# Kernel optimization log

Measured on AMD Instinct MI355X. Metric: run time of the kernel, lower is better.

Reference implementation:

```python
import jax, jax.numpy as jnp
import numpy as np

L, B, S, D, H, F = 4, 8, 512, 512, 8, 2048
KS = (1, 3, 5)
DEPTH = D // H


def causal_conv(x, W, b):
    # x: [B,S,D], W: [k,D,D] (WIO), causal left pad k-1
    k = W.shape[0]
    y = jax.lax.conv_general_dilated(x, W, (1,), [(k - 1, 0)],
                                     dimension_numbers=('NWC', 'WIO', 'NWC'))
    return y + b


def layer_norm(x, g, b, eps=1e-6):
    mu = jnp.mean(x, -1, keepdims=True)
    var = jnp.mean((x - mu) ** 2, -1, keepdims=True)
    return (x - mu) * jax.lax.rsqrt(var + eps) * g + b


def split_heads(t):
    return t.reshape(B, S, H, DEPTH).transpose(0, 2, 1, 3)  # [B,H,S,depth]


def setup_inputs() -> dict:
    key = jax.random.key(0)
    keys = iter(jax.random.split(key, 16))
    rn = lambda shape, s=0.02: jax.random.normal(next(keys), shape, jnp.float32) * s
    inp = {"x": jax.random.normal(next(keys), (B, S, D), jnp.float32)}
    for k in KS:
        inp[f"Wq{k}"] = rn((L, k, D, D))
        inp[f"Wk{k}"] = rn((L, k, D, D))
    inp["bq"] = jnp.zeros((L, 3, D), jnp.float32)
    inp["bk"] = jnp.zeros((L, 3, D), jnp.float32)
    inp["Wv"] = rn((L, 3, 1, D, D))
    inp["bv"] = jnp.zeros((L, 3, D), jnp.float32)
    inp["Wo"] = rn((L, D, D)); inp["bo"] = jnp.zeros((L, D), jnp.float32)
    inp["W1"] = rn((L, D, F)); inp["b1"] = jnp.zeros((L, F), jnp.float32)
    inp["W2"] = rn((L, F, D)); inp["b2"] = jnp.zeros((L, D), jnp.float32)
    inp["ln1_g"] = jnp.ones((L, D), jnp.float32); inp["ln1_b"] = jnp.zeros((L, D), jnp.float32)
    inp["ln2_g"] = jnp.ones((L, D), jnp.float32); inp["ln2_b"] = jnp.zeros((L, D), jnp.float32)
    return inp


def reference(x, Wq1, Wq3, Wq5, Wk1, Wk3, Wk5, bq, bk, Wv, bv, Wo, bo,
              W1, b1, W2, b2, ln1_g, ln1_b, ln2_g, ln2_b):
    # causal look-ahead mask: 1 - band_part(ones, -1, 0), added as mask * -1e9
    neg_mask = (1.0 - jnp.tril(jnp.ones((S, S), jnp.float32))) * -1e9
    scale = 1.0 / jnp.sqrt(jnp.float32(DEPTH))
    Wqs, Wks = (Wq1, Wq3, Wq5), (Wk1, Wk3, Wk5)
    for l in range(L):
        outs = []
        for i in range(len(KS)):
            q = split_heads(causal_conv(x, Wqs[i][l], bq[l, i]))
            k = split_heads(causal_conv(x, Wks[i][l], bk[l, i]))
            v = split_heads(causal_conv(x, Wv[l, i], bv[l, i]))
            logits = jnp.einsum('bhqd,bhkd->bhqk', q, k) * scale + neg_mask
            a = jax.nn.softmax(logits, axis=-1)
            o = jnp.einsum('bhqk,bhkd->bhqd', a, v)
            outs.append(o.transpose(0, 2, 1, 3).reshape(B, S, D))
        attn_out = ((outs[0] + outs[1] + outs[2]) / 3.0) @ Wo[l] + bo[l]
        out1 = layer_norm(attn_out + x, ln1_g[l], ln1_b[l])
        ffn = jax.nn.relu(out1 @ W1[l] + b1[l]) @ W2[l] + b2[l]
        x = layer_norm(ffn + out1, ln2_g[l], ln2_b[l])
    return x
```

## Files before the change

kernel.cpp:

```cpp
#include <hip/hip_runtime.h>
#include <cstdint>
#include <cstddef>

#define Dm 512
#define Sm 512
#define Bm 8
#define Hm 8
#define Fm 2048
#define Mm 4096
#define Lm 4

typedef __bf16 bf16x8 __attribute__((ext_vector_type(8)));
typedef float  fx4    __attribute__((ext_vector_type(4)));
typedef float  fx2    __attribute__((ext_vector_type(2)));
typedef unsigned short u16;
typedef unsigned short u16x4 __attribute__((ext_vector_type(4)));
typedef short s16x8 __attribute__((ext_vector_type(8)));

__device__ __forceinline__ u16 f2b(float f) {
  union { float f; uint32_t u; } v; v.f = f;
  uint32_t u = v.u;
  return (u16)((u + 0x7fffu + ((u >> 16) & 1u)) >> 16);
}
__device__ __forceinline__ float b2f(u16 h) {
  union { uint32_t u; float f; } v; v.u = ((uint32_t)h) << 16;
  return v.f;
}

__device__ __forceinline__ void gload16(const void* g, void* l) {
  __builtin_amdgcn_global_load_lds(
      (const __attribute__((address_space(1))) void*)g,
      (__attribute__((address_space(3))) void*)l, 16, 0, 0);
}

__global__ void cast_bf16_kernel(const float* __restrict__ in, u16* __restrict__ out,
                                 u16* __restrict__ zpad) {
  int i = (blockIdx.x * 256 + threadIdx.x) * 4;
  fx4 v = *(const fx4*)(in + i);
  u16x4 o;
  #pragma unroll
  for (int j = 0; j < 4; ++j) o[j] = f2b(v[j]);
  *(u16x4*)(out + i) = o;
  if (blockIdx.x == 0) { zpad[threadIdx.x] = 0; zpad[threadIdx.x + 256] = 0; }
}

__global__ void avg3_kernel(const u16* __restrict__ o3, u16* __restrict__ out) {
  int i = (blockIdx.x * 256 + threadIdx.x) * 4;
  u16x4 a = *(const u16x4*)(o3 + i);
  u16x4 b = *(const u16x4*)(o3 + (size_t)Mm*Dm + i);
  u16x4 c = *(const u16x4*)(o3 + (size_t)2*Mm*Dm + i);
  u16x4 r;
  #pragma unroll
  for (int j = 0; j < 4; ++j)
    r[j] = f2b((b2f(a[j]) + b2f(b[j]) + b2f(c[j])) * (1.f/3.f));
  *(u16x4*)(out + i) = r;
}

__global__ void ln_kernel(const float* __restrict__ in, const float* __restrict__ gam,
                          const float* __restrict__ bet, float* __restrict__ outf,
                          u16* __restrict__ outb) {
  int row = blockIdx.x;
  int t = threadIdx.x;
  const float* x = in + (size_t)row * Dm;
  fx4 v0 = *(const fx4*)(x + t*4);
  fx4 v1 = *(const fx4*)(x + 256 + t*4);
  float s = 0.f, sq = 0.f;
  #pragma unroll
  for (int j = 0; j < 4; ++j) { s += v0[j] + v1[j]; sq += v0[j]*v0[j] + v1[j]*v1[j]; }
  #pragma unroll
  for (int off = 1; off < 64; off <<= 1) { s += __shfl_xor(s, off, 64); sq += __shfl_xor(sq, off, 64); }
  float mu  = s * (1.f/Dm);
  float var = sq * (1.f/Dm) - mu*mu;
  float rstd = rsqrtf(var + 1e-6f);
  fx4 g0 = *(const fx4*)(gam + t*4), g1 = *(const fx4*)(gam + 256 + t*4);
  fx4 b0 = *(const fx4*)(bet + t*4), b1 = *(const fx4*)(bet + 256 + t*4);
  float* of = outf + (size_t)row*Dm;
  u16*   ob = outb + (size_t)row*Dm;
  fx4 y0, y1; u16x4 h0, h1;
  #pragma unroll
  for (int j = 0; j < 4; ++j) {
    y0[j] = (v0[j]-mu)*rstd*g0[j] + b0[j];
    y1[j] = (v1[j]-mu)*rstd*g1[j] + b1[j];
    h0[j] = f2b(y0[j]); h1[j] = f2b(y1[j]);
  }
  *(fx4*)(of + t*4) = y0; *(fx4*)(of + 256 + t*4) = y1;
  *(u16x4*)(ob + t*4) = h0; *(u16x4*)(ob + 256 + t*4) = h1;
}

#define TST 130
__global__ void prep_kernel(u16* __restrict__ packed,
    const float* __restrict__ Wq1, const float* __restrict__ Wq3, const float* __restrict__ Wq5,
    const float* __restrict__ Wk1, const float* __restrict__ Wk3, const float* __restrict__ Wk5,
    const float* __restrict__ Wv,  const float* __restrict__ Wo,
    const float* __restrict__ W1,  const float* __restrict__ W2, int layer) {
  __shared__ float T[64 * TST];
  constexpr int t0[13] = {0,32,128,288,320,416,576,608,640,672,704,832,960};
  int bid = blockIdx.x;
  int seg = 0;
  while (bid >= t0[seg+1]) ++seg;
  int local = bid - t0[seg];
  const float* src; int K, N;
  switch (seg) {
    case 0:  src = Wq1 + (size_t)layer*512*512;   K = 512;  N = 512;  break;
    case 1:  src = Wq3 + (size_t)layer*3*512*512; K = 1536; N = 512;  break;
    case 2:  src = Wq5 + (size_t)layer*5*512*512; K = 2560; N = 512;  break;
    case 3:  src = Wk1 + (size_t)layer*512*512;   K = 512;  N = 512;  break;
    case 4:  src = Wk3 + (size_t)layer*3*512*512; K = 1536; N = 512;  break;
    case 5:  src = Wk5 + (size_t)layer*5*512*512; K = 2560; N = 512;  break;
    case 6:  src = Wv + (size_t)(layer*3+0)*512*512; K = 512; N = 512; break;
    case 7:  src = Wv + (size_t)(layer*3+1)*512*512; K = 512; N = 512; break;
    case 8:  src = Wv + (size_t)(layer*3+2)*512*512; K = 512; N = 512; break;
    case 9:  src = Wo + (size_t)layer*512*512;    K = 512;  N = 512;  break;
    case 10: src = W1 + (size_t)layer*512*2048;   K = 512;  N = 2048; break;
    default: src = W2 + (size_t)layer*2048*512;   K = 2048; N = 512;  break;
  }
  int KT = K >> 6;
  int ntile = local / KT, ktile = local - ntile*KT;
  const float* sb = src + (size_t)(ktile*64)*N + ntile*128;
  int tid = threadIdx.x;
  #pragma unroll
  for (int i = 0; i < 16; ++i) {
    int idx = i*256 + tid;
    int row = idx >> 6, col2 = (idx & 63) * 2;
    fx2 v = *(const fx2*)(sb + (size_t)row*N + col2);
    *(fx2*)(&T[row*TST + col2]) = v;
  }
  __syncthreads();
  u16* dst = packed + ((size_t)bid << 13);
  #pragma unroll
  for (int j = 0; j < 4; ++j) {
    int z = j*256 + tid;
    int row = z >> 3;
    int c = (z & 7) ^ (row & 7);
    s16x8 o;
    #pragma unroll
    for (int e = 0; e < 8; ++e) o[e] = (short)f2b(T[(c*8 + e)*TST + row]);
    *(s16x8*)(dst + z*8) = o;
  }
}

__global__ __launch_bounds__(256, 2) void conv_all(const u16* __restrict__ xb,
    const u16* __restrict__ packed,
    const float* __restrict__ bq, const float* __restrict__ bk, const float* __restrict__ bv,
    u16* __restrict__ qb, u16* __restrict__ kb, u16* __restrict__ vT, int layer,
    const u16* __restrict__ zpad) {
  __shared__ __align__(16) u16 As[2][8192];
  __shared__ __align__(16) u16 Bs[2][8192];
  constexpr int t0c[9]   = {0,32,128,288,320,416,576,608,640};
  constexpr int tapsc[9] = {1,3,5,1,3,5,1,1,1};
  constexpr int order[9] = {2,5,1,4,0,3,6,7,8};
  int bid = blockIdx.x;
  int unit = order[bid >> 7];
  int local = bid & 127;
  int mtile = local >> 2, ntile = local & 3;
  int taps = tapsc[unit];
  int brow = mtile * 128, bcol = ntile * 128;
  int tid = threadIdx.x, lane = tid & 63, wid = tid >> 6;
  int wm = wid >> 1, wn = wid & 1;
  int r16 = lane & 15, g = lane >> 4;
  int tbase = t0c[unit] + ntile * taps * 8;
  fx4 acc[4][4] = {};
  int ntiles = taps * 8;
  int st = 0, skt = 0, sidx = 0;
  auto stage = [&](int bufi) {
    int shift = taps - 1 - st;
    int c0 = skt << 6;
    #pragma unroll
    for (int j = 0; j < 4; ++j) {
      int zb = wid*256 + j*64;
      int zz = zb + lane;
      int row = zz >> 3, c = (zz & 7) ^ (row & 7);
      int s = (brow + row) & (Sm - 1);
      const u16* src = (s >= shift) ? (xb + (size_t)(brow + row - shift)*Dm + c0 + c*8) : zpad;
      gload16(src, &As[bufi][zb * 8]);
    }
    const u16* wt = packed + ((size_t)(tbase + sidx) << 13);
    #pragma unroll
    for (int j = 0; j < 4; ++j) {
      int zb = wid*256 + j*64;
      gload16(wt + (size_t)(zb + lane)*8, &Bs[bufi][zb * 8]);
    }
  };
  stage(0);
  ++skt; ++sidx; if (skt == 8) { skt = 0; ++st; }
  __syncthreads();
  for (int idx = 0; idx < ntiles; ++idx) {
    int cur = idx & 1;
    if (idx + 1 < ntiles) {
      stage(cur ^ 1);
      ++skt; ++sidx; if (skt == 8) { skt = 0; ++st; }
    }
    bf16x8 a[2][4], b[2][4];
    #pragma unroll
    for (int kk = 0; kk < 2; ++kk) {
      #pragma unroll
      for (int m = 0; m < 4; ++m) {
        int row = wm*64 + m*16 + r16;
        a[kk][m] = *(const bf16x8*)(&As[cur][(row << 6) + (((kk*4 + g) ^ (row & 7)) << 3)]);
      }
      #pragma unroll
      for (int n = 0; n < 4; ++n) {
        int row = wn*64 + n*16 + r16;
        b[kk][n] = *(const bf16x8*)(&Bs[cur][(row << 6) + (((kk*4 + g) ^ (row & 7)) << 3)]);
      }
    }
    #pragma unroll
    for (int kk = 0; kk < 2; ++kk)
      #pragma unroll
      for (int m = 0; m < 4; ++m)
        #pragma unroll
        for (int n = 0; n < 4; ++n)
          acc[m][n] = __builtin_amdgcn_mfma_f32_16x16x32_bf16(a[kk][m], b[kk][n], acc[m][n], 0, 0, 0);
    __syncthreads();
  }
  const float* bias; u16* outp;
  if (unit < 3)      { bias = bq + (size_t)(layer*3 + unit)*Dm;   outp = qb + (size_t)unit*Mm*Dm; }
  else if (unit < 6) { bias = bk + (size_t)(layer*3 + unit-3)*Dm; outp = kb + (size_t)(unit-3)*Mm*Dm; }
  else               { bias = bv + (size_t)(layer*3 + unit-6)*Dm; outp = vT + ((size_t)(unit-6) << 21); }
  if (unit < 6) {
    #pragma unroll
    for (int m = 0; m < 4; ++m) {
      int row0 = brow + wm*64 + m*16 + g*4;
      #pragma unroll
      for (int n = 0; n < 4; ++n) {
        int col = bcol + wn*64 + n*16 + r16;
        float bv_ = bias[col];
        #pragma unroll
        for (int r = 0; r < 4; ++r)
          outp[(size_t)(row0 + r)*Dm + col] = f2b(acc[m][n][r] + bv_);
      }
    }
  } else {
    #pragma unroll
    for (int m = 0; m < 4; ++m) {
      int row0 = brow + wm*64 + m*16 + g*4;
      int bidx = row0 >> 9, spos = row0 & 511;
      #pragma unroll
      for (int n = 0; n < 4; ++n) {
        int col = bcol + wn*64 + n*16 + r16;
        int hh = col >> 6, dd = col & 63;
        float bv_ = bias[col];
        u16x4 pk;
        #pragma unroll
        for (int r = 0; r < 4; ++r) pk[r] = f2b(acc[m][n][r] + bv_);
        *(u16x4*)(outp + (((size_t)(bidx*8 + hh)*64 + dd) << 9) + spos) = pk;
      }
    }
  }
}

template<int MODE, int BMt, int WN, bool CAUSAL>
__device__ __forceinline__ void gemm_core(const u16* __restrict__ A, int lda, int Ktap, int taps,
    const u16* __restrict__ Wt, const float* __restrict__ bias, const float* __restrict__ res,
    u16* __restrict__ outb, float* __restrict__ outf, int N, const u16* __restrict__ zpad) {
  constexpr int NR = 128 / (16 * WN);
  __shared__ __align__(16) u16 As[2][BMt * 64];
  __shared__ __align__(16) u16 Bs[2][8192];
  int tid = threadIdx.x, lane = tid & 63, wid = tid >> 6;
  int wm = (WN == 2) ? (wid >> 1) : 0;
  int wn = (WN == 2) ? (wid & 1) : wid;
  int r16 = lane & 15, g = lane >> 4;
  int brow = blockIdx.x * BMt, bcol = blockIdx.y * 128;
  int KT = Ktap >> 6;
  const u16* WtN = Wt + ((size_t)(blockIdx.y * taps * KT) << 13);
  fx4 acc[4][NR] = {};
  int ntiles = taps * KT;
  int st = 0, skt = 0, sidx = 0;
  auto stage = [&](int bufi) {
    int shift = taps - 1 - st;
    int c0 = skt << 6;
    #pragma unroll
    for (int j = 0; j < BMt/32; ++j) {
      int zb = wid*(BMt*2) + j*64;
      int zz = zb + lane;
      int row = zz >> 3, c = (zz & 7) ^ (row & 7);
      const u16* src;
      if (CAUSAL) {
        int s = (brow + row) & (Sm - 1);
        src = (s >= shift) ? (A + (size_t)(brow + row - shift)*lda + c0 + c*8) : zpad;
      } else {
        src = A + (size_t)(brow + row)*lda + c0 + c*8;
      }
      gload16(src, &As[bufi][zb * 8]);
    }
    const u16* wt = WtN + ((size_t)sidx << 13);
    #pragma unroll
    for (int j = 0; j < 4; ++j) {
      int zb = wid*256 + j*64;
      gload16(wt + (size_t)(zb + lane)*8, &Bs[bufi][zb * 8]);
    }
  };
  stage(0);
  ++skt; ++sidx; if (skt == KT) { skt = 0; ++st; }
  __syncthreads();
  for (int idx = 0; idx < ntiles; ++idx) {
    int cur = idx & 1;
    if (idx + 1 < ntiles) {
      stage(cur ^ 1);
      ++skt; ++sidx; if (skt == KT) { skt = 0; ++st; }
    }
    bf16x8 a[2][4], b[2][NR];
    #pragma unroll
    for (int kk = 0; kk < 2; ++kk) {
      #pragma unroll
      for (int m = 0; m < 4; ++m) {
        int row = wm*64 + m*16 + r16;
        a[kk][m] = *(const bf16x8*)(&As[cur][(row << 6) + (((kk*4 + g) ^ (row & 7)) << 3)]);
      }
      #pragma unroll
      for (int n = 0; n < NR; ++n) {
        int row = wn*(NR*16) + n*16 + r16;
        b[kk][n] = *(const bf16x8*)(&Bs[cur][(row << 6) + (((kk*4 + g) ^ (row & 7)) << 3)]);
      }
    }
    #pragma unroll
    for (int kk = 0; kk < 2; ++kk)
      #pragma unroll
      for (int m = 0; m < 4; ++m)
        #pragma unroll
        for (int n = 0; n < NR; ++n)
          acc[m][n] = __builtin_amdgcn_mfma_f32_16x16x32_bf16(a[kk][m], b[kk][n], acc[m][n], 0, 0, 0);
    __syncthreads();
  }
  #pragma unroll
  for (int m = 0; m < 4; ++m) {
    int row0 = brow + wm*64 + m*16 + g*4;
    #pragma unroll
    for (int n = 0; n < NR; ++n) {
      int col = bcol + wn*(NR*16) + n*16 + r16;
      float bv_ = bias[col];
      #pragma unroll
      for (int r = 0; r < 4; ++r) {
        size_t idx = (size_t)(row0 + r)*N + col;
        float v = acc[m][n][r] + bv_;
        if (MODE == 0)      outb[idx] = f2b(v);
        else if (MODE == 1) outb[idx] = f2b(fmaxf(v, 0.f));
        else                outf[idx] = v + res[idx];
      }
    }
  }
}

template<int MODE, int BMt, int WN, int LB>
__global__ __launch_bounds__(256, LB) void gemm_dense(const u16* __restrict__ A, int lda, int K,
    const u16* __restrict__ Wt, const float* __restrict__ bias, const float* __restrict__ res,
    u16* __restrict__ outb, float* __restrict__ outf, int N) {
  gemm_core<MODE, BMt, WN, false>(A, lda, K, 1, Wt, bias, res, outb, outf, N, nullptr);
}

__global__ __launch_bounds__(256, 3) void attn_kernel(const u16* __restrict__ qb,
    const u16* __restrict__ kb, const u16* __restrict__ vTb, u16* __restrict__ ob) {
  __shared__ __align__(16) u16 Ks[2][4096];
  __shared__ __align__(16) u16 Vs[2][4096];
  __shared__ __align__(16) u16 Ps[4][1024];
  int a = blockIdx.x, bh = blockIdx.y, br = blockIdx.z;
  int b = bh >> 3, h = bh & 7;
  const u16* q  = qb + (size_t)br*Mm*Dm;
  const u16* k  = kb + (size_t)br*Mm*Dm;
  const u16* vT = vTb + (((size_t)br << 21) + ((size_t)bh << 15));
  u16* o = ob + (size_t)br*Mm*Dm;
  int tid = threadIdx.x, lane = tid & 63, wid = tid >> 6;
  int r16 = lane & 15, g = lane >> 4;
  size_t rowbase = (size_t)b * Sm;
  int qt[2] = {7 - a, a};
  int nkt = qt[0] + 1;

  bf16x8 qa[2][2];
  #pragma unroll
  for (int t2 = 0; t2 < 2; ++t2)
    #pragma unroll
    for (int c = 0; c < 2; ++c)
      qa[t2][c] = *(const bf16x8*)(q + (rowbase + qt[t2]*64 + wid*16 + r16)*Dm + h*64 + c*32 + g*8);

  float m_[2][4], l_[2][4];
  fx4 accO[2][4] = {};
  #pragma unroll
  for (int t2 = 0; t2 < 2; ++t2)
    #pragma unroll
    for (int r = 0; r < 4; ++r) { m_[t2][r] = -3.0e38f; l_[t2][r] = 0.f; }

  auto stage = [&](int kt, int bufi) {
    #pragma unroll
    for (int it = 0; it < 2; ++it) {
      int zb = wid*128 + it*64;
      int zz = zb + lane;
      int row = zz >> 3, c = (zz & 7) ^ (row & 7);
      gload16(k + (rowbase + kt*64 + row)*Dm + h*64 + c*8, &Ks[bufi][zb * 8]);
      gload16(vT + ((size_t)row << 9) + kt*64 + c*8, &Vs[bufi][zb * 8]);
    }
  };
  stage(0, 0);
  __syncthreads();

  for (int kt = 0; kt < nkt; ++kt) {
    int cur = kt & 1;
    if (kt + 1 < nkt) stage(kt + 1, cur ^ 1);
    #pragma unroll
    for (int t2 = 0; t2 < 2; ++t2) {
      if (t2 == 0 || kt <= qt[1]) {
        fx4 sacc[4] = {};
        #pragma unroll
        for (int c = 0; c < 2; ++c)
          #pragma unroll
          for (int n = 0; n < 4; ++n) {
            int row = n*16 + r16;
            bf16x8 kf = *(const bf16x8*)(&Ks[cur][(row << 6) + (((c*4 + g) ^ (row & 7)) << 3)]);
            sacc[n] = __builtin_amdgcn_mfma_f32_16x16x32_bf16(qa[t2][c], kf, sacc[n], 0, 0, 0);
          }
        float sv[4][4];
        bool diag = (kt == qt[t2]);
        #pragma unroll
        for (int n = 0; n < 4; ++n)
          #pragma unroll
          for (int r = 0; r < 4; ++r) {
            float s = sacc[n][r] * 0.125f;
            if (diag && (n*16 + r16 > wid*16 + g*4 + r)) s = -3.0e38f;
            sv[n][r] = s;
          }
        #pragma unroll
        for (int r = 0; r < 4; ++r) {
          float rm = fmaxf(fmaxf(sv[0][r], sv[1][r]), fmaxf(sv[2][r], sv[3][r]));
          #pragma unroll
          for (int off = 1; off < 16; off <<= 1) rm = fmaxf(rm, __shfl_xor(rm, off, 64));
          float mnew = fmaxf(m_[t2][r], rm);
          float corr = __expf(m_[t2][r] - mnew);
          m_[t2][r] = mnew;
          float rs = 0.f;
          #pragma unroll
          for (int n = 0; n < 4; ++n) { float p = __expf(sv[n][r] - mnew); sv[n][r] = p; rs += p; }
          #pragma unroll
          for (int off = 1; off < 16; off <<= 1) rs += __shfl_xor(rs, off, 64);
          l_[t2][r] = l_[t2][r]*corr + rs;
          #pragma unroll
          for (int n = 0; n < 4; ++n) accO[t2][n][r] *= corr;
        }
        #pragma unroll
        for (int n = 0; n < 4; ++n)
          #pragma unroll
          for (int r = 0; r < 4; ++r) {
            int qq = g*4 + r;
            Ps[wid][(qq << 6) + (((n*2 + (r16 >> 3)) ^ (qq & 7)) << 3) + (r16 & 7)] = f2b(sv[n][r]);
          }
        #pragma unroll
        for (int kk = 0; kk < 2; ++kk) {
          bf16x8 pa = *(const bf16x8*)(&Ps[wid][(r16 << 6) + (((kk*4 + g) ^ (r16 & 7)) << 3)]);
          #pragma unroll
          for (int n = 0; n < 4; ++n) {
            int row = n*16 + r16;
            bf16x8 vf = *(const bf16x8*)(&Vs[cur][(row << 6) + (((kk*4 + g) ^ (row & 7)) << 3)]);
            accO[t2][n] = __builtin_amdgcn_mfma_f32_16x16x32_bf16(pa, vf, accO[t2][n], 0, 0, 0);
          }
        }
      }
    }
    __syncthreads();
  }
  #pragma unroll
  for (int t2 = 0; t2 < 2; ++t2)
    #pragma unroll
    for (int n = 0; n < 4; ++n)
      #pragma unroll
      for (int r = 0; r < 4; ++r) {
        int qrow = qt[t2]*64 + wid*16 + g*4 + r;
        o[(rowbase + qrow)*Dm + h*64 + n*16 + r16] = f2b(accO[t2][n][r] / l_[t2][r]);
      }
}

extern "C" void kernel_launch(void* const* d_in, const int* in_sizes, int n_in,
                              void* d_out, int out_size, void* d_ws, size_t ws_size,
                              hipStream_t stream) {
  const float* x_in = (const float*)d_in[0];
  const float* Wq1 = (const float*)d_in[1];
  const float* Wk1 = (const float*)d_in[2];
  const float* Wq3 = (const float*)d_in[3];
  const float* Wk3 = (const float*)d_in[4];
  const float* Wq5 = (const float*)d_in[5];
  const float* Wk5 = (const float*)d_in[6];
  const float* bq  = (const float*)d_in[7];
  const float* bk  = (const float*)d_in[8];
  const float* Wv  = (const float*)d_in[9];
  const float* bv  = (const float*)d_in[10];
  const float* Wo  = (const float*)d_in[11];
  const float* bo  = (const float*)d_in[12];
  const float* W1  = (const float*)d_in[13];
  const float* b1  = (const float*)d_in[14];
  const float* W2  = (const float*)d_in[15];
  const float* b2  = (const float*)d_in[16];
  const float* ln1g = (const float*)d_in[17];
  const float* ln1b = (const float*)d_in[18];
  const float* ln2g = (const float*)d_in[19];
  const float* ln2b = (const float*)d_in[20];

  char* ws = (char*)d_ws;
  size_t off = 0;
  auto alloc = [&](size_t bytes) { void* p = ws + off; off += (bytes + 255) & ~(size_t)255; return p; };
  float* x_f32 = (float*)alloc((size_t)Mm*Dm*4);
  u16*   xb    = (u16*)  alloc((size_t)Mm*Dm*2);
  u16*   qbuf  = (u16*)  alloc((size_t)3*Mm*Dm*2);
  u16*   kbuf  = (u16*)  alloc((size_t)3*Mm*Dm*2);
  u16*   vT    = (u16*)  alloc((size_t)3*Mm*Dm*2);
  u16*   obuf  = (u16*)  alloc((size_t)3*Mm*Dm*2);
  u16*   avgb  = (u16*)  alloc((size_t)Mm*Dm*2);
  float* pre   = (float*)alloc((size_t)Mm*Dm*4);
  float* out1f = (float*)alloc((size_t)Mm*Dm*4);
  u16*   out1b = (u16*)  alloc((size_t)Mm*Dm*2);
  u16*   midb  = (u16*)  alloc((size_t)Mm*Fm*2);
  u16*   packed= (u16*)  alloc((size_t)960*8192*2);
  u16*   zpad  = (u16*)  alloc(1024);

  cast_bf16_kernel<<<2048, 256, 0, stream>>>(x_in, xb, zpad);
  for (int l = 0; l < Lm; ++l) {
    const float* xs = (l == 0) ? x_in : x_f32;
    prep_kernel<<<960, 256, 0, stream>>>(packed, Wq1, Wq3, Wq5, Wk1, Wk3, Wk5,
                                         Wv, Wo, W1, W2, l);
    conv_all<<<1152, 256, 0, stream>>>(
        xb, packed, bq, bk, bv, qbuf, kbuf, vT, l, zpad);
    attn_kernel<<<dim3(4, 64, 3), 256, 0, stream>>>(qbuf, kbuf, vT, obuf);
    avg3_kernel<<<2048, 256, 0, stream>>>(obuf, avgb);
    gemm_dense<2, 64, 4, 3><<<dim3(64, 4), 256, 0, stream>>>(
        avgb, 512, 512, packed + ((size_t)672 << 13), bo + (size_t)l*Dm, xs, nullptr, pre, 512);
    ln_kernel<<<4096, 64, 0, stream>>>(pre, ln1g + (size_t)l*Dm, ln1b + (size_t)l*Dm, out1f, out1b);
    gemm_dense<1, 128, 2, 2><<<dim3(32, 16), 256, 0, stream>>>(
        out1b, 512, 512, packed + ((size_t)704 << 13), b1 + (size_t)l*Fm, nullptr, midb, nullptr, 2048);
    gemm_dense<2, 64, 4, 3><<<dim3(64, 4), 256, 0, stream>>>(
        midb, 2048, 2048, packed + ((size_t)832 << 13), b2 + (size_t)l*Dm, out1f, nullptr, pre, 512);
    float* lnout = (l == Lm-1) ? (float*)d_out : x_f32;
    ln_kernel<<<4096, 64, 0, stream>>>(pre, ln2g + (size_t)l*Dm, ln2b + (size_t)l*Dm, lnout, xb);
  }
}
```

Measured before the change: 649.2 us.

## Read weight tiles straight from global memory and split FFN2 K across two partial outputs

The conv and GEMM kernels no longer stage the packed weight (B) tiles through shared memory. Each wave loads its B fragments directly from global memory, relying on cache reuse. This halves LDS use so occupancy can rise, and the launch bounds move to 3 blocks per SM. The FFN2 GEMM is split-K into two halves written to separate fp32 buffers, which the following LayerNorm sums, doubling grid size. The risk is global-load latency on B that is no longer hidden by a double buffer, plus extra fp32 traffic for the second partial buffer.

Measured after the change: 671.4 us. +3.4%, slower.

```diff
diff --git a/kernel.cpp b/kernel.cpp
--- a/kernel.cpp
+++ b/kernel.cpp
@@ -34,7 +34,7 @@
 }
 
 __global__ void cast_bf16_kernel(const float* __restrict__ in, u16* __restrict__ out,
-                                 u16* __restrict__ zpad) {
+                                 u16* __restrict__ zpad, float* __restrict__ zerof) {
   int i = (blockIdx.x * 256 + threadIdx.x) * 4;
   fx4 v = *(const fx4*)(in + i);
   u16x4 o;
@@ -42,6 +42,10 @@
   for (int j = 0; j < 4; ++j) o[j] = f2b(v[j]);
   *(u16x4*)(out + i) = o;
   if (blockIdx.x == 0) { zpad[threadIdx.x] = 0; zpad[threadIdx.x + 256] = 0; }
+  if (blockIdx.x == 1) {
+    #pragma unroll
+    for (int j = 0; j < 8; ++j) zerof[threadIdx.x * 8 + j] = 0.f;
+  }
 }
 
 __global__ void avg3_kernel(const u16* __restrict__ o3, u16* __restrict__ out) {
@@ -56,14 +60,21 @@
   *(u16x4*)(out + i) = r;
 }
 
-__global__ void ln_kernel(const float* __restrict__ in, const float* __restrict__ gam,
-                          const float* __restrict__ bet, float* __restrict__ outf,
-                          u16* __restrict__ outb) {
+__global__ void ln_kernel(const float* __restrict__ in, const float* __restrict__ in2,
+                          const float* __restrict__ gam, const float* __restrict__ bet,
+                          float* __restrict__ outf, u16* __restrict__ outb) {
   int row = blockIdx.x;
   int t = threadIdx.x;
   const float* x = in + (size_t)row * Dm;
   fx4 v0 = *(const fx4*)(x + t*4);
   fx4 v1 = *(const fx4*)(x + 256 + t*4);
+  if (in2) {
+    const float* x2 = in2 + (size_t)row * Dm;
+    fx4 w0 = *(const fx4*)(x2 + t*4);
+    fx4 w1 = *(const fx4*)(x2 + 256 + t*4);
+    #pragma unroll
+    for (int j = 0; j < 4; ++j) { v0[j] += w0[j]; v1[j] += w1[j]; }
+  }
   float s = 0.f, sq = 0.f;
   #pragma unroll
   for (int j = 0; j < 4; ++j) { s += v0[j] + v1[j]; sq += v0[j]*v0[j] + v1[j]*v1[j]; }
@@ -139,13 +150,12 @@
   }
 }
 
-__global__ __launch_bounds__(256, 2) void conv_all(const u16* __restrict__ xb,
+__global__ __launch_bounds__(256, 3) void conv_all(const u16* __restrict__ xb,
     const u16* __restrict__ packed,
     const float* __restrict__ bq, const float* __restrict__ bk, const float* __restrict__ bv,
     u16* __restrict__ qb, u16* __restrict__ kb, u16* __restrict__ vT, int layer,
     const u16* __restrict__ zpad) {
   __shared__ __align__(16) u16 As[2][8192];
-  __shared__ __align__(16) u16 Bs[2][8192];
   constexpr int t0c[9]   = {0,32,128,288,320,416,576,608,640};
   constexpr int tapsc[9] = {1,3,5,1,3,5,1,1,1};
   constexpr int order[9] = {2,5,1,4,0,3,6,7,8};
@@ -161,8 +171,8 @@
   int tbase = t0c[unit] + ntile * taps * 8;
   fx4 acc[4][4] = {};
   int ntiles = taps * 8;
-  int st = 0, skt = 0, sidx = 0;
-  auto stage = [&](int bufi) {
+  int st = 0, skt = 0;
+  auto stageA = [&](int bufi) {
     int shift = taps - 1 - st;
     int c0 = skt << 6;
     #pragma unroll
@@ -174,36 +184,33 @@
       const u16* src = (s >= shift) ? (xb + (size_t)(brow + row - shift)*Dm + c0 + c*8) : zpad;
       gload16(src, &As[bufi][zb * 8]);
     }
-    const u16* wt = packed + ((size_t)(tbase + sidx) << 13);
-    #pragma unroll
-    for (int j = 0; j < 4; ++j) {
-      int zb = wid*256 + j*64;
-      gload16(wt + (size_t)(zb + lane)*8, &Bs[bufi][zb * 8]);
-    }
   };
-  stage(0);
-  ++skt; ++sidx; if (skt == 8) { skt = 0; ++st; }
+  stageA(0);
+  ++skt; if (skt == 8) { skt = 0; ++st; }
   __syncthreads();
   for (int idx = 0; idx < ntiles; ++idx) {
     int cur = idx & 1;
+    const u16* wtc = packed + ((size_t)(tbase + idx) << 13);
+    bf16x8 b[2][4];
+    #pragma unroll
+    for (int kk = 0; kk < 2; ++kk)
+      #pragma unroll
+      for (int n = 0; n < 4; ++n) {
+        int row = wn*64 + n*16 + r16;
+        b[kk][n] = *(const bf16x8*)(wtc + (row << 6) + (((kk*4 + g) ^ (row & 7)) << 3));
+      }
     if (idx + 1 < ntiles) {
-      stage(cur ^ 1);
-      ++skt; ++sidx; if (skt == 8) { skt = 0; ++st; }
-    }
-    bf16x8 a[2][4], b[2][4];
-    #pragma unroll
-    for (int kk = 0; kk < 2; ++kk) {
+      stageA(cur ^ 1);
+      ++skt; if (skt == 8) { skt = 0; ++st; }
+    }
+    bf16x8 a[2][4];
+    #pragma unroll
+    for (int kk = 0; kk < 2; ++kk)
       #pragma unroll
       for (int m = 0; m < 4; ++m) {
         int row = wm*64 + m*16 + r16;
         a[kk][m] = *(const bf16x8*)(&As[cur][(row << 6) + (((kk*4 + g) ^ (row & 7)) << 3)]);
       }
-      #pragma unroll
-      for (int n = 0; n < 4; ++n) {
-        int row = wn*64 + n*16 + r16;
-        b[kk][n] = *(const bf16x8*)(&Bs[cur][(row << 6) + (((kk*4 + g) ^ (row & 7)) << 3)]);
-      }
-    }
     #pragma unroll
     for (int kk = 0; kk < 2; ++kk)
       #pragma unroll
@@ -252,21 +259,21 @@
 template<int MODE, int BMt, int WN, bool CAUSAL>
 __device__ __forceinline__ void gemm_core(const u16* __restrict__ A, int lda, int Ktap, int taps,
     const u16* __restrict__ Wt, const float* __restrict__ bias, const float* __restrict__ res,
-    u16* __restrict__ outb, float* __restrict__ outf, int N, const u16* __restrict__ zpad) {
+    u16* __restrict__ outb, float* __restrict__ outf, int N, const u16* __restrict__ zpad,
+    int ktN_stride, int ktile0) {
   constexpr int NR = 128 / (16 * WN);
   __shared__ __align__(16) u16 As[2][BMt * 64];
-  __shared__ __align__(16) u16 Bs[2][8192];
   int tid = threadIdx.x, lane = tid & 63, wid = tid >> 6;
   int wm = (WN == 2) ? (wid >> 1) : 0;
   int wn = (WN == 2) ? (wid & 1) : wid;
   int r16 = lane & 15, g = lane >> 4;
   int brow = blockIdx.x * BMt, bcol = blockIdx.y * 128;
   int KT = Ktap >> 6;
-  const u16* WtN = Wt + ((size_t)(blockIdx.y * taps * KT) << 13);
+  const u16* WtN = Wt + ((size_t)(blockIdx.y * ktN_stride + ktile0) << 13);
   fx4 acc[4][NR] = {};
   int ntiles = taps * KT;
-  int st = 0, skt = 0, sidx = 0;
-  auto stage = [&](int bufi) {
+  int st = 0, skt = 0;
+  auto stageA = [&](int bufi) {
     int shift = taps - 1 - st;
     int c0 = skt << 6;
     #pragma unroll
@@ -283,36 +290,33 @@
       }
       gload16(src, &As[bufi][zb * 8]);
     }
-    const u16* wt = WtN + ((size_t)sidx << 13);
-    #pragma unroll
-    for (int j = 0; j < 4; ++j) {
-      int zb = wid*256 + j*64;
-      gload16(wt + (size_t)(zb + lane)*8, &Bs[bufi][zb * 8]);
-    }
   };
-  stage(0);
-  ++skt; ++sidx; if (skt == KT) { skt = 0; ++st; }
+  stageA(0);
+  ++skt; if (skt == KT) { skt = 0; ++st; }
   __syncthreads();
   for (int idx = 0; idx < ntiles; ++idx) {
     int cur = idx & 1;
+    const u16* wtc = WtN + ((size_t)idx << 13);
+    bf16x8 b[2][NR];
+    #pragma unroll
+    for (int kk = 0; kk < 2; ++kk)
+      #pragma unroll
+      for (int n = 0; n < NR; ++n) {
+        int row = wn*(NR*16) + n*16 + r16;
+        b[kk][n] = *(const bf16x8*)(wtc + (row << 6) + (((kk*4 + g) ^ (row & 7)) << 3));
+      }
     if (idx + 1 < ntiles) {
-      stage(cur ^ 1);
-      ++skt; ++sidx; if (skt == KT) { skt = 0; ++st; }
-    }
-    bf16x8 a[2][4], b[2][NR];
-    #pragma unroll
-    for (int kk = 0; kk < 2; ++kk) {
+      stageA(cur ^ 1);
+      ++skt; if (skt == KT) { skt = 0; ++st; }
+    }
+    bf16x8 a[2][4];
+    #pragma unroll
+    for (int kk = 0; kk < 2; ++kk)
       #pragma unroll
       for (int m = 0; m < 4; ++m) {
         int row = wm*64 + m*16 + r16;
         a[kk][m] = *(const bf16x8*)(&As[cur][(row << 6) + (((kk*4 + g) ^ (row & 7)) << 3)]);
       }
-      #pragma unroll
-      for (int n = 0; n < NR; ++n) {
-        int row = wn*(NR*16) + n*16 + r16;
-        b[kk][n] = *(const bf16x8*)(&Bs[cur][(row << 6) + (((kk*4 + g) ^ (row & 7)) << 3)]);
-      }
-    }
     #pragma unroll
     for (int kk = 0; kk < 2; ++kk)
       #pragma unroll
@@ -335,7 +339,7 @@
         float v = acc[m][n][r] + bv_;
         if (MODE == 0)      outb[idx] = f2b(v);
         else if (MODE == 1) outb[idx] = f2b(fmaxf(v, 0.f));
-        else                outf[idx] = v + res[idx];
+        else                outf[idx] = v + (res ? res[idx] : 0.f);
       }
     }
   }
@@ -345,7 +349,15 @@
 __global__ __launch_bounds__(256, LB) void gemm_dense(const u16* __restrict__ A, int lda, int K,
     const u16* __restrict__ Wt, const float* __restrict__ bias, const float* __restrict__ res,
     u16* __restrict__ outb, float* __restrict__ outf, int N) {
-  gemm_core<MODE, BMt, WN, false>(A, lda, K, 1, Wt, bias, res, outb, outf, N, nullptr);
+  gemm_core<MODE, BMt, WN, false>(A, lda, K, 1, Wt, bias, res, outb, outf, N, nullptr, K >> 6, 0);
+}
+
+__global__ __launch_bounds__(256, 3) void gemm_ffn2(const u16* __restrict__ A,
+    const u16* __restrict__ Wt, const float* __restrict__ bias, const float* __restrict__ zerof,
+    const float* __restrict__ res, float* __restrict__ pre, float* __restrict__ pre2) {
+  int z = blockIdx.z;
+  gemm_core<2, 64, 4, false>(A + z*1024, 2048, 1024, 1, Wt,
+      z ? zerof : bias, z ? nullptr : res, nullptr, z ? pre2 : pre, 512, nullptr, 32, z*16);
 }
 
 __global__ __launch_bounds__(256, 3) void attn_kernel(const u16* __restrict__ qb,
@@ -502,13 +514,15 @@
   u16*   obuf  = (u16*)  alloc((size_t)3*Mm*Dm*2);
   u16*   avgb  = (u16*)  alloc((size_t)Mm*Dm*2);
   float* pre   = (float*)alloc((size_t)Mm*Dm*4);
+  float* pre2  = (float*)alloc((size_t)Mm*Dm*4);
   float* out1f = (float*)alloc((size_t)Mm*Dm*4);
   u16*   out1b = (u16*)  alloc((size_t)Mm*Dm*2);
   u16*   midb  = (u16*)  alloc((size_t)Mm*Fm*2);
   u16*   packed= (u16*)  alloc((size_t)960*8192*2);
   u16*   zpad  = (u16*)  alloc(1024);
-
-  cast_bf16_kernel<<<2048, 256, 0, stream>>>(x_in, xb, zpad);
+  float* zerof = (float*)alloc(2048*4);
+
+  cast_bf16_kernel<<<2048, 256, 0, stream>>>(x_in, xb, zpad, zerof);
   for (int l = 0; l < Lm; ++l) {
     const float* xs = (l == 0) ? x_in : x_f32;
     prep_kernel<<<960, 256, 0, stream>>>(packed, Wq1, Wq3, Wq5, Wk1, Wk3, Wk5,
@@ -519,12 +533,14 @@
     avg3_kernel<<<2048, 256, 0, stream>>>(obuf, avgb);
     gemm_dense<2, 64, 4, 3><<<dim3(64, 4), 256, 0, stream>>>(
         avgb, 512, 512, packed + ((size_t)672 << 13), bo + (size_t)l*Dm, xs, nullptr, pre, 512);
-    ln_kernel<<<4096, 64, 0, stream>>>(pre, ln1g + (size_t)l*Dm, ln1b + (size_t)l*Dm, out1f, out1b);
-    gemm_dense<1, 128, 2, 2><<<dim3(32, 16), 256, 0, stream>>>(
+    ln_kernel<<<4096, 64, 0, stream>>>(pre, nullptr, ln1g + (size_t)l*Dm, ln1b + (size_t)l*Dm,
+                                       out1f, out1b);
+    gemm_dense<1, 128, 2, 3><<<dim3(32, 16), 256, 0, stream>>>(
         out1b, 512, 512, packed + ((size_t)704 << 13), b1 + (size_t)l*Fm, nullptr, midb, nullptr, 2048);
-    gemm_dense<2, 64, 4, 3><<<dim3(64, 4), 256, 0, stream>>>(
-        midb, 2048, 2048, packed + ((size_t)832 << 13), b2 + (size_t)l*Dm, out1f, nullptr, pre, 512);
+    gemm_ffn2<<<dim3(64, 4, 2), 256, 0, stream>>>(
+        midb, packed + ((size_t)832 << 13), b2 + (size_t)l*Dm, zerof, out1f, pre, pre2);
     float* lnout = (l == Lm-1) ? (float*)d_out : x_f32;
-    ln_kernel<<<4096, 64, 0, stream>>>(pre, ln2g + (size_t)l*Dm, ln2b + (size_t)l*Dm, lnout, xb);
-  }
-}
+    ln_kernel<<<4096, 64, 0, stream>>>(pre, pre2, ln2g + (size_t)l*Dm, ln2b + (size_t)l*Dm,
+                                       lnout, xb);
+  }
+}
```

## Load GEMM weight fragments directly into registers, bypassing LDS, with register double-buffering

Applied to the files above, without the earlier changes.

Both the conv_all kernel and the shared GEMM core stop staging the pre-packed weight tiles through shared memory. Each wave now reads its swizzled weight fragments straight from global memory into two register buffers that alternate between K steps. Only the activation tile still goes through LDS, and an explicit vmcnt wait plus s_barrier replaces __syncthreads. MFMA blocks are also wrapped in s_setprio. This halves LDS traffic and footprint, which may help occupancy, but waves that share weight columns now load duplicate fragments from global/L2, and register pressure rises.

After: 620.4 us. 4.4% less time.

```diff
diff --git a/kernel.cpp b/kernel.cpp
--- a/kernel.cpp
+++ b/kernel.cpp
@@ -31,6 +31,13 @@
   __builtin_amdgcn_global_load_lds(
       (const __attribute__((address_space(1))) void*)g,
       (__attribute__((address_space(3))) void*)l, 16, 0, 0);
+}
+
+template<int N>
+__device__ __forceinline__ void vwait() {
+  if constexpr (N == 4)      asm volatile("s_waitcnt vmcnt(4)" ::: "memory");
+  else if constexpr (N == 8) asm volatile("s_waitcnt vmcnt(8)" ::: "memory");
+  else                       asm volatile("s_waitcnt vmcnt(0)" ::: "memory");
 }
 
 __global__ void cast_bf16_kernel(const float* __restrict__ in, u16* __restrict__ out,
@@ -139,13 +146,48 @@
   }
 }
 
+#define GEMM_STEP(IDX, CB, NB, BC, BN, NRv, NW)                                   \
+  {                                                                              \
+    bool hn = (IDX) + 1 < ntiles;                                                \
+    if (hn) {                                                                    \
+      stageA(NB);                                                                \
+      ++skt; if (skt == KTt) { skt = 0; ++st; }                                  \
+      const u16* wtn = WtN + ((size_t)((IDX) + 1) << 13);                        \
+      _Pragma("unroll")                                                          \
+      for (int kk = 0; kk < 2; ++kk)                                             \
+        _Pragma("unroll")                                                        \
+        for (int n = 0; n < NRv; ++n) {                                          \
+          int row = wn*(NRv*16) + n*16 + r16;                                    \
+          BN[kk][n] = *(const bf16x8*)(wtn + (row << 6) + (((kk*4 + g) ^ (row & 7)) << 3)); \
+        }                                                                        \
+    }                                                                            \
+    bf16x8 a_[2][4];                                                             \
+    _Pragma("unroll")                                                            \
+    for (int kk = 0; kk < 2; ++kk)                                               \
+      _Pragma("unroll")                                                          \
+      for (int m = 0; m < 4; ++m) {                                              \
+        int row = wm*64 + m*16 + r16;                                            \
+        a_[kk][m] = *(const bf16x8*)(&As[CB][(row << 6) + (((kk*4 + g) ^ (row & 7)) << 3)]); \
+      }                                                                          \
+    __builtin_amdgcn_s_setprio(1);                                               \
+    _Pragma("unroll")                                                            \
+    for (int kk = 0; kk < 2; ++kk)                                               \
+      _Pragma("unroll")                                                          \
+      for (int m = 0; m < 4; ++m)                                                \
+        _Pragma("unroll")                                                        \
+        for (int n = 0; n < NRv; ++n)                                            \
+          acc[m][n] = __builtin_amdgcn_mfma_f32_16x16x32_bf16(a_[kk][m], BC[kk][n], acc[m][n], 0, 0, 0); \
+    __builtin_amdgcn_s_setprio(0);                                               \
+    vwait<2*NRv>();                                                              \
+    __builtin_amdgcn_s_barrier();                                                \
+  }
+
 __global__ __launch_bounds__(256, 2) void conv_all(const u16* __restrict__ xb,
     const u16* __restrict__ packed,
     const float* __restrict__ bq, const float* __restrict__ bk, const float* __restrict__ bv,
     u16* __restrict__ qb, u16* __restrict__ kb, u16* __restrict__ vT, int layer,
     const u16* __restrict__ zpad) {
   __shared__ __align__(16) u16 As[2][8192];
-  __shared__ __align__(16) u16 Bs[2][8192];
   constexpr int t0c[9]   = {0,32,128,288,320,416,576,608,640};
   constexpr int tapsc[9] = {1,3,5,1,3,5,1,1,1};
   constexpr int order[9] = {2,5,1,4,0,3,6,7,8};
@@ -158,11 +200,12 @@
   int tid = threadIdx.x, lane = tid & 63, wid = tid >> 6;
   int wm = wid >> 1, wn = wid & 1;
   int r16 = lane & 15, g = lane >> 4;
-  int tbase = t0c[unit] + ntile * taps * 8;
+  const u16* WtN = packed + ((size_t)(t0c[unit] + ntile * taps * 8) << 13);
   fx4 acc[4][4] = {};
   int ntiles = taps * 8;
-  int st = 0, skt = 0, sidx = 0;
-  auto stage = [&](int bufi) {
+  const int KTt = 8;
+  int st = 0, skt = 0;
+  auto stageA = [&](int bufi) {
     int shift = taps - 1 - st;
     int c0 = skt << 6;
     #pragma unroll
@@ -174,44 +217,21 @@
       const u16* src = (s >= shift) ? (xb + (size_t)(brow + row - shift)*Dm + c0 + c*8) : zpad;
       gload16(src, &As[bufi][zb * 8]);
     }
-    const u16* wt = packed + ((size_t)(tbase + sidx) << 13);
-    #pragma unroll
-    for (int j = 0; j < 4; ++j) {
-      int zb = wid*256 + j*64;
-      gload16(wt + (size_t)(zb + lane)*8, &Bs[bufi][zb * 8]);
-    }
   };
-  stage(0);
-  ++skt; ++sidx; if (skt == 8) { skt = 0; ++st; }
+  bf16x8 bA[2][4], bB[2][4];
+  stageA(0);
+  ++skt; if (skt == KTt) { skt = 0; ++st; }
+  #pragma unroll
+  for (int kk = 0; kk < 2; ++kk)
+    #pragma unroll
+    for (int n = 0; n < 4; ++n) {
+      int row = wn*64 + n*16 + r16;
+      bA[kk][n] = *(const bf16x8*)(WtN + (row << 6) + (((kk*4 + g) ^ (row & 7)) << 3));
+    }
   __syncthreads();
-  for (int idx = 0; idx < ntiles; ++idx) {
-    int cur = idx & 1;
-    if (idx + 1 < ntiles) {
-      stage(cur ^ 1);
-      ++skt; ++sidx; if (skt == 8) { skt = 0; ++st; }
-    }
-    bf16x8 a[2][4], b[2][4];
-    #pragma unroll
-    for (int kk = 0; kk < 2; ++kk) {
-      #pragma unroll
-      for (int m = 0; m < 4; ++m) {
-        int row = wm*64 + m*16 + r16;
-        a[kk][m] = *(const bf16x8*)(&As[cur][(row << 6) + (((kk*4 + g) ^ (row & 7)) << 3)]);
-      }
-      #pragma unroll
-      for (int n = 0; n < 4; ++n) {
-        int row = wn*64 + n*16 + r16;
-        b[kk][n] = *(const bf16x8*)(&Bs[cur][(row << 6) + (((kk*4 + g) ^ (row & 7)) << 3)]);
-      }
-    }
-    #pragma unroll
-    for (int kk = 0; kk < 2; ++kk)
-      #pragma unroll
-      for (int m = 0; m < 4; ++m)
-        #pragma unroll
-        for (int n = 0; n < 4; ++n)
-          acc[m][n] = __builtin_amdgcn_mfma_f32_16x16x32_bf16(a[kk][m], b[kk][n], acc[m][n], 0, 0, 0);
-    __syncthreads();
+  for (int base = 0; base < ntiles; base += 2) {
+    GEMM_STEP(base,     0, 1, bA, bB, 4, 2)
+    GEMM_STEP(base + 1, 1, 0, bB, bA, 4, 2)
   }
   const float* bias; u16* outp;
   if (unit < 3)      { bias = bq + (size_t)(layer*3 + unit)*Dm;   outp = qb + (size_t)unit*Mm*Dm; }
@@ -254,23 +274,23 @@
     const u16* __restrict__ Wt, const float* __restrict__ bias, const float* __restrict__ res,
     u16* __restrict__ outb, float* __restrict__ outf, int N, const u16* __restrict__ zpad) {
   constexpr int NR = 128 / (16 * WN);
+  constexpr int AD = BMt / 32;
   __shared__ __align__(16) u16 As[2][BMt * 64];
-  __shared__ __align__(16) u16 Bs[2][8192];
   int tid = threadIdx.x, lane = tid & 63, wid = tid >> 6;
   int wm = (WN == 2) ? (wid >> 1) : 0;
   int wn = (WN == 2) ? (wid & 1) : wid;
   int r16 = lane & 15, g = lane >> 4;
   int brow = blockIdx.x * BMt, bcol = blockIdx.y * 128;
-  int KT = Ktap >> 6;
-  const u16* WtN = Wt + ((size_t)(blockIdx.y * taps * KT) << 13);
+  const int KTt = Ktap >> 6;
+  const u16* WtN = Wt + ((size_t)(blockIdx.y * taps * KTt) << 13);
   fx4 acc[4][NR] = {};
-  int ntiles = taps * KT;
-  int st = 0, skt = 0, sidx = 0;
-  auto stage = [&](int bufi) {
+  int ntiles = taps * KTt;
+  int st = 0, skt = 0;
+  auto stageA = [&](int bufi) {
     int shift = taps - 1 - st;
     int c0 = skt << 6;
     #pragma unroll
-    for (int j = 0; j < BMt/32; ++j) {
+    for (int j = 0; j < AD; ++j) {
       int zb = wid*(BMt*2) + j*64;
       int zz = zb + lane;
       int row = zz >> 3, c = (zz & 7) ^ (row & 7);
@@ -283,44 +303,21 @@
       }
       gload16(src, &As[bufi][zb * 8]);
     }
-    const u16* wt = WtN + ((size_t)sidx << 13);
-    #pragma unroll
-    for (int j = 0; j < 4; ++j) {
-      int zb = wid*256 + j*64;
-      gload16(wt + (size_t)(zb + lane)*8, &Bs[bufi][zb * 8]);
-    }
   };
-  stage(0);
-  ++skt; ++sidx; if (skt == KT) { skt = 0; ++st; }
+  bf16x8 bA[2][NR], bB[2][NR];
+  stageA(0);
+  ++skt; if (skt == KTt) { skt = 0; ++st; }
+  #pragma unroll
+  for (int kk = 0; kk < 2; ++kk)
+    #pragma unroll
+    for (int n = 0; n < NR; ++n) {
+      int row = wn*(NR*16) + n*16 + r16;
+      bA[kk][n] = *(const bf16x8*)(WtN + (row << 6) + (((kk*4 + g) ^ (row & 7)) << 3));
+    }
   __syncthreads();
-  for (int idx = 0; idx < ntiles; ++idx) {
-    int cur = idx & 1;
-    if (idx + 1 < ntiles) {
-      stage(cur ^ 1);
-      ++skt; ++sidx; if (skt == KT) { skt = 0; ++st; }
-    }
-    bf16x8 a[2][4], b[2][NR];
-    #pragma unroll
-    for (int kk = 0; kk < 2; ++kk) {
-      #pragma unroll
-      for (int m = 0; m < 4; ++m) {
-        int row = wm*64 + m*16 + r16;
-        a[kk][m] = *(const bf16x8*)(&As[cur][(row << 6) + (((kk*4 + g) ^ (row & 7)) << 3)]);
-      }
-      #pragma unroll
-      for (int n = 0; n < NR; ++n) {
-        int row = wn*(NR*16) + n*16 + r16;
-        b[kk][n] = *(const bf16x8*)(&Bs[cur][(row << 6) + (((kk*4 + g) ^ (row & 7)) << 3)]);
-      }
-    }
-    #pragma unroll
-    for (int kk = 0; kk < 2; ++kk)
-      #pragma unroll
-      for (int m = 0; m < 4; ++m)
-        #pragma unroll
-        for (int n = 0; n < NR; ++n)
-          acc[m][n] = __builtin_amdgcn_mfma_f32_16x16x32_bf16(a[kk][m], b[kk][n], acc[m][n], 0, 0, 0);
-    __syncthreads();
+  for (int base = 0; base < ntiles; base += 2) {
+    GEMM_STEP(base,     0, 1, bA, bB, NR, WN)
+    GEMM_STEP(base + 1, 1, 0, bB, bA, NR, WN)
   }
   #pragma unroll
   for (int m = 0; m < 4; ++m) {
```
